# Kernel optimization log

Measured on AMD Instinct MI355X. Metric: run time of the kernel, lower is better.

The kernel has to match this reference:

```python
import jax, jax.numpy as jnp
import numpy as np

T, B, N_INP, N_HID, N_OUT = 512, 128, 256, 1024, 128


def setup_inputs() -> dict:
    key = jax.random.key(0)
    ks = jax.random.split(key, 7)
    x = jax.random.normal(ks[0], (T, B, N_INP), dtype=jnp.float32)
    # PyTorch RNNCell/Linear default init: U(-1/sqrt(fan_in), 1/sqrt(fan_in))
    s_h = 1.0 / np.sqrt(N_HID)
    W_ih = jax.random.uniform(ks[1], (N_HID, N_INP), jnp.float32, -s_h, s_h)
    W_hh = jax.random.uniform(ks[2], (N_HID, N_HID), jnp.float32, -s_h, s_h)
    b_ih = jax.random.uniform(ks[3], (N_HID,), jnp.float32, -s_h, s_h)
    b_hh = jax.random.uniform(ks[4], (N_HID,), jnp.float32, -s_h, s_h)
    W_ro = jax.random.uniform(ks[5], (N_OUT, N_HID), jnp.float32, -s_h, s_h)
    b_ro = jax.random.uniform(ks[6], (N_OUT,), jnp.float32, -s_h, s_h)
    return {"x": x, "W_ih": W_ih, "W_hh": W_hh, "b_ih": b_ih,
            "b_hh": b_hh, "W_ro": W_ro, "b_ro": b_ro}


def reference(x, W_ih, W_hh, b_ih, b_hh, W_ro, b_ro):
    # x: [T, B, n_inp]; recurrence: state = tanh(x_t W_ih^T + b_ih + state W_hh^T + b_hh)
    batch = x.shape[1]
    n_hid = W_hh.shape[0]
    state0 = jnp.zeros((batch, n_hid), dtype=x.dtype)

    # Precompute the input projection for all timesteps in one big GEMM.
    x_proj = jnp.einsum('tbi,hi->tbh', x, W_ih) + b_ih + b_hh  # [T, B, n_hid]

    def step(state, xp_t):
        new_state = jnp.tanh(xp_t + state @ W_hh.T)
        return new_state, None

    final_state, _ = jax.lax.scan(step, state0, x_proj)
    # readout applied to final hidden state only (stateOnly=None path)
    return final_state @ W_ro.T + b_ro  # [B, n_out]
```

## Files before the change

### kernel.cpp

```cpp
#include <hip/hip_runtime.h>
#include <hip/hip_bf16.h>
#include <stdint.h>


#define TSTEPS 512
#define BATCH  128
#define NI     256
#define NH     1024
#define NO     128
#define NBLK   64
#define NTHR   512
#define NWAVE  8
#define BG     16
#define COLS   128

typedef __attribute__((ext_vector_type(8))) short s16x8;
typedef __attribute__((ext_vector_type(4))) float f32x4;
typedef __attribute__((ext_vector_type(4))) unsigned u32x4;
typedef unsigned long long ull;

__device__ __forceinline__ unsigned short f2bf_rne(float f) {
  unsigned u = __builtin_bit_cast(unsigned, f);
  unsigned r = u + 0x7fffu + ((u >> 16) & 1u);
  return (unsigned short)(r >> 16);
}
__device__ __forceinline__ float bf2f(unsigned short h) {
  unsigned u = ((unsigned)h) << 16;
  return __builtin_bit_cast(float, u);
}
__device__ __forceinline__ void split_bf(float v, short &hi, short &lo) {
  unsigned short h = f2bf_rne(v);
  hi = (short)h;
  lo = (short)f2bf_rne(v - bf2f(h));
}
__device__ __forceinline__ f32x4 mfma16(s16x8 a, s16x8 b, f32x4 c) {
  return __builtin_amdgcn_mfma_f32_16x16x32_bf16(a, b, c, 0, 0, 0);
}
__device__ __forceinline__ float fast_tanh(float a) {
  float cl = fminf(fmaxf(a, -15.f), 15.f);
  float e  = __expf(2.f * cl);
  return (e - 1.f) / (e + 1.f);
}

#define SIDX(g, p, r, k) ((((size_t)(g) * NWAVE + (p)) * BG + (r)) * 128 + (k))

__global__ __launch_bounds__(NTHR, 2)
void rnn_persistent(const float* __restrict__ x,
                    const float* __restrict__ W_ih,
                    const float* __restrict__ W_hh,
                    const float* __restrict__ b_ih,
                    const float* __restrict__ b_hh,
                    unsigned*    __restrict__ SP)
{
  const int tid  = threadIdx.x;
  const int wave = tid >> 6;
  const int lane = tid & 63;
  const int lr   = lane & 15;
  const int lq   = lane >> 4;
  const int g    = blockIdx.x & 7;
  const int p    = blockIdx.x >> 3;
  const int row0 = g * BG;
  const int h0   = p * COLS;
  const int kq0  = wave * 128;
  const int iq0  = wave * 32;

  __shared__ float red[NWAVE][BG][COLS];

  s16x8 whh[8][4];
  #pragma unroll
  for (int nt = 0; nt < 8; ++nt) {
    const int h = h0 + nt * 16 + lr;
    #pragma unroll
    for (int kb = 0; kb < 4; ++kb) {
      const float* pw = W_hh + (size_t)h * NH + kq0 + kb * 32 + lq * 8;
      s16x8 hi;
      #pragma unroll
      for (int j = 0; j < 8; ++j) hi[j] = (short)f2bf_rne(pw[j]);
      whh[nt][kb] = hi;
    }
  }
  s16x8 wih[8];
  #pragma unroll
  for (int nt = 0; nt < 8; ++nt) {
    const int h = h0 + nt * 16 + lr;
    const float* pw = W_ih + (size_t)h * NI + iq0 + lq * 8;
    s16x8 hi;
    #pragma unroll
    for (int j = 0; j < 8; ++j) hi[j] = (short)f2bf_rne(pw[j]);
    wih[nt] = hi;
  }

  const int er = tid >> 5;
  const int ec = (tid & 31) * 4;
  float bias[4];
  #pragma unroll
  for (int j = 0; j < 4; ++j) bias[j] = b_ih[h0 + ec + j] + b_hh[h0 + ec + j];

  unsigned* buf0 = SP;
  unsigned* buf1 = SP + (size_t)BATCH * NH;

  float xf[8];
  {
    const float* xp = x + (size_t)(row0 + lr) * NI + iq0 + lq * 8;
    #pragma unroll
    for (int j = 0; j < 8; ++j) xf[j] = xp[j];
  }

  const unsigned* sb0 = buf0 + SIDX(g, wave, lr, lq * 8);
  const unsigned* sb1 = buf1 + SIDX(g, wave, lr, lq * 8);

  for (int t = 0; t < TSTEPS; ++t) {
    f32x4 acc[8];
    #pragma unroll
    for (int nt = 0; nt < 8; ++nt) acc[nt] = (f32x4){0.f, 0.f, 0.f, 0.f};
    {
      s16x8 xhi, xlo;
      #pragma unroll
      for (int j = 0; j < 8; ++j) { short a, b; split_bf(xf[j], a, b); xhi[j] = a; xlo[j] = b; }
      #pragma unroll
      for (int nt = 0; nt < 8; ++nt) {
        acc[nt] = mfma16(xhi, wih[nt], acc[nt]);
        acc[nt] = mfma16(xlo, wih[nt], acc[nt]);
      }
    }
    const unsigned etag = (unsigned)((t >> 1) & 1);
    const unsigned* sb = (t & 1) ? sb1 : sb0;
    u32x4 sv0, sv1, sv2, sv3, sv4, sv5, sv6, sv7;
    {
      const u32x4 e4 = (u32x4){etag, etag, etag, etag};
      for (;;) {
        asm volatile(
          "global_load_dwordx4 %0, %8, off sc1\n\t"
          "global_load_dwordx4 %1, %8, off offset:16 sc1\n\t"
          "global_load_dwordx4 %2, %8, off offset:128 sc1\n\t"
          "global_load_dwordx4 %3, %8, off offset:144 sc1\n\t"
          "global_load_dwordx4 %4, %8, off offset:256 sc1\n\t"
          "global_load_dwordx4 %5, %8, off offset:272 sc1\n\t"
          "global_load_dwordx4 %6, %8, off offset:384 sc1\n\t"
          "global_load_dwordx4 %7, %8, off offset:400 sc1\n\t"
          "s_waitcnt vmcnt(0)"
          : "=&v"(sv0), "=&v"(sv1), "=&v"(sv2), "=&v"(sv3),
            "=&v"(sv4), "=&v"(sv5), "=&v"(sv6), "=&v"(sv7)
          : "v"(sb) : "memory");
        u32x4 b4 = (sv0 ^ e4) | (sv1 ^ e4) | (sv2 ^ e4) | (sv3 ^ e4)
                 | (sv4 ^ e4) | (sv5 ^ e4) | (sv6 ^ e4) | (sv7 ^ e4);
        unsigned bad = b4[0] | b4[1] | b4[2] | b4[3];
        if ((bad & 1u) == 0) break;
      }
    }
    {
      const int tn = (t + 1 < TSTEPS) ? (t + 1) : t;
      const float* xp = x + (size_t)tn * BATCH * NI + (size_t)(row0 + lr) * NI + iq0 + lq * 8;
      #pragma unroll
      for (int j = 0; j < 8; ++j) xf[j] = xp[j];
    }
    #pragma unroll
    for (int kb = 0; kb < 4; ++kb) {
      const u32x4 va = (kb == 0) ? sv0 : (kb == 1) ? sv2 : (kb == 2) ? sv4 : sv6;
      const u32x4 vb = (kb == 0) ? sv1 : (kb == 1) ? sv3 : (kb == 2) ? sv5 : sv7;
      s16x8 shi, slo;
      #pragma unroll
      for (int i = 0; i < 4; ++i) {
        unsigned wa = va[i], wb = vb[i];
        shi[i]     = (short)(wa >> 16); slo[i]     = (short)(wa & 0xffffu);
        shi[i + 4] = (short)(wb >> 16); slo[i + 4] = (short)(wb & 0xffffu);
      }
      #pragma unroll
      for (int nt = 0; nt < 8; ++nt) {
        acc[nt] = mfma16(shi, whh[nt][kb], acc[nt]);
        acc[nt] = mfma16(slo, whh[nt][kb], acc[nt]);
      }
    }
    __syncthreads();
    #pragma unroll
    for (int nt = 0; nt < 8; ++nt)
      #pragma unroll
      for (int r = 0; r < 4; ++r)
        red[wave][lq * 4 + r][nt * 16 + lr] = acc[nt][r];
    __syncthreads();
    {
      float s[4] = {bias[0], bias[1], bias[2], bias[3]};
      #pragma unroll
      for (int w = 0; w < NWAVE; ++w) {
        const f32x4 v = *(const f32x4*)&red[w][er][ec];
        s[0] += v[0]; s[1] += v[1]; s[2] += v[2]; s[3] += v[3];
      }
      const unsigned otag = (unsigned)(((t + 1) >> 1) & 1);
      unsigned pkw[4];
      #pragma unroll
      for (int j = 0; j < 4; ++j) {
        float tv = fast_tanh(s[j]);
        unsigned short hb = f2bf_rne(tv);
        unsigned       lb = ((f2bf_rne(tv - bf2f(hb)) & 0xfffeu) | otag);
        pkw[j] = (((unsigned)hb) << 16) | lb;
      }
      ull pk01 = ((ull)pkw[1] << 32) | (ull)pkw[0];
      ull pk23 = ((ull)pkw[3] << 32) | (ull)pkw[2];
      ull* op = (ull*)(((t + 1) & 1 ? buf1 : buf0) + SIDX(g, p, er, ec));
      __hip_atomic_store(op,     pk01, __ATOMIC_RELAXED, __HIP_MEMORY_SCOPE_AGENT);
      __hip_atomic_store(op + 1, pk23, __ATOMIC_RELAXED, __HIP_MEMORY_SCOPE_AGENT);
    }
  }
}

__global__ __launch_bounds__(256)
void init_buf1(unsigned* __restrict__ SP) {
  const int i = blockIdx.x * 256 + threadIdx.x;
  SP[BATCH * NH + i] = 1u;
}

__global__ __launch_bounds__(512)
void rnn_readout(const unsigned* __restrict__ SP,
                 const float* __restrict__ W_ro,
                 const float* __restrict__ b_ro,
                 float* __restrict__ out)
{
  __shared__ float srow[4][NH];
  const int b0 = blockIdx.x * 4;
  for (int i = threadIdx.x; i < 4 * NH; i += 512) {
    const int b = b0 + (i >> 10);
    const int h = i & 1023;
    unsigned u = SP[SIDX(b >> 4, h >> 7, b & 15, h & 127)];
    srow[i >> 10][h] = bf2f((unsigned short)(u >> 16)) + bf2f((unsigned short)(u & 0xffffu));
  }
  __syncthreads();
  const int bb = threadIdx.x >> 7;
  const int o  = threadIdx.x & 127;
  const float* wr = W_ro + (size_t)o * NH;
  float s = 0.f;
  #pragma unroll 4
  for (int k = 0; k < NH; ++k) s += srow[bb][k] * wr[k];
  out[(size_t)(b0 + bb) * NO + o] = s + b_ro[o];
}

extern "C" void kernel_launch(void* const* d_in, const int* in_sizes, int n_in,
                              void* d_out, int out_size, void* d_ws, size_t ws_size,
                              hipStream_t stream) {
  (void)in_sizes; (void)n_in; (void)out_size; (void)ws_size;
  const float* x    = (const float*)d_in[0];
  const float* W_ih = (const float*)d_in[1];
  const float* W_hh = (const float*)d_in[2];
  const float* b_ih = (const float*)d_in[3];
  const float* b_hh = (const float*)d_in[4];
  const float* W_ro = (const float*)d_in[5];
  const float* b_ro = (const float*)d_in[6];
  float* out = (float*)d_out;

  unsigned* SP = (unsigned*)d_ws;

  hipMemsetAsync(SP, 0, (size_t)BATCH * NH * sizeof(unsigned), stream);
  init_buf1<<<(BATCH * NH) / 256, 256, 0, stream>>>(SP);

  rnn_persistent<<<NBLK, NTHR, 0, stream>>>(x, W_ih, W_hh, b_ih, b_hh, SP);
  rnn_readout<<<BATCH / 4, 512, 0, stream>>>(SP, W_ro, b_ro, out);
}
```

Before: 2.177 ms.

## Mirror hidden state into two buffers with different cache scopes for faster polling

Result: slower. 2.444 ms (+12.3%).

```diff
diff --git a/kernel.cpp b/kernel.cpp
--- a/kernel.cpp
+++ b/kernel.cpp
@@ -13,6 +13,7 @@
 #define NWAVE  8
 #define BG     16
 #define COLS   128
+#define SPBUF  ((size_t)BATCH * NH)
 
 typedef __attribute__((ext_vector_type(8))) short s16x8;
 typedef __attribute__((ext_vector_type(4))) float f32x4;
@@ -44,7 +45,7 @@
 
 #define SIDX(g, p, r, k) ((((size_t)(g) * NWAVE + (p)) * BG + (r)) * 128 + (k))
 
-__global__ __launch_bounds__(NTHR, 2)
+__global__ __launch_bounds__(NTHR, 1)
 void rnn_persistent(const float* __restrict__ x,
                     const float* __restrict__ W_ih,
                     const float* __restrict__ W_hh,
@@ -96,8 +97,10 @@
   #pragma unroll
   for (int j = 0; j < 4; ++j) bias[j] = b_ih[h0 + ec + j] + b_hh[h0 + ec + j];
 
-  unsigned* buf0 = SP;
-  unsigned* buf1 = SP + (size_t)BATCH * NH;
+  unsigned* lb0 = SP;
+  unsigned* lb1 = SP + SPBUF;
+  unsigned* mr0 = SP + 2 * SPBUF;
+  unsigned* mr1 = SP + 3 * SPBUF;
 
   float xf[8];
   {
@@ -106,8 +109,10 @@
     for (int j = 0; j < 8; ++j) xf[j] = xp[j];
   }
 
-  const unsigned* sb0 = buf0 + SIDX(g, wave, lr, lq * 8);
-  const unsigned* sb1 = buf1 + SIDX(g, wave, lr, lq * 8);
+  const size_t soff = SIDX(g, wave, lr, lq * 8);
+  const unsigned* sbL[2] = { lb0 + soff, lb1 + soff };
+  const unsigned* sbM[2] = { mr0 + soff, mr1 + soff };
+  const size_t poff = SIDX(g, p, er, ec);
 
   for (int t = 0; t < TSTEPS; ++t) {
     f32x4 acc[8];
@@ -124,11 +129,31 @@
       }
     }
     const unsigned etag = (unsigned)((t >> 1) & 1);
-    const unsigned* sb = (t & 1) ? sb1 : sb0;
+    const unsigned* sb = sbL[t & 1];
+    const unsigned* mb = sbM[t & 1];
     u32x4 sv0, sv1, sv2, sv3, sv4, sv5, sv6, sv7;
     {
       const u32x4 e4 = (u32x4){etag, etag, etag, etag};
       for (;;) {
+        asm volatile(
+          "global_load_dwordx4 %0, %8, off sc0\n\t"
+          "global_load_dwordx4 %1, %8, off offset:16 sc0\n\t"
+          "global_load_dwordx4 %2, %8, off offset:128 sc0\n\t"
+          "global_load_dwordx4 %3, %8, off offset:144 sc0\n\t"
+          "global_load_dwordx4 %4, %8, off offset:256 sc0\n\t"
+          "global_load_dwordx4 %5, %8, off offset:272 sc0\n\t"
+          "global_load_dwordx4 %6, %8, off offset:384 sc0\n\t"
+          "global_load_dwordx4 %7, %8, off offset:400 sc0\n\t"
+          "s_waitcnt vmcnt(0)"
+          : "=&v"(sv0), "=&v"(sv1), "=&v"(sv2), "=&v"(sv3),
+            "=&v"(sv4), "=&v"(sv5), "=&v"(sv6), "=&v"(sv7)
+          : "v"(sb) : "memory");
+        {
+          u32x4 b4 = (sv0 ^ e4) | (sv1 ^ e4) | (sv2 ^ e4) | (sv3 ^ e4)
+                   | (sv4 ^ e4) | (sv5 ^ e4) | (sv6 ^ e4) | (sv7 ^ e4);
+          unsigned bad = b4[0] | b4[1] | b4[2] | b4[3];
+          if ((bad & 1u) == 0) break;
+        }
         asm volatile(
           "global_load_dwordx4 %0, %8, off sc1\n\t"
           "global_load_dwordx4 %1, %8, off offset:16 sc1\n\t"
@@ -141,11 +166,13 @@
           "s_waitcnt vmcnt(0)"
           : "=&v"(sv0), "=&v"(sv1), "=&v"(sv2), "=&v"(sv3),
             "=&v"(sv4), "=&v"(sv5), "=&v"(sv6), "=&v"(sv7)
-          : "v"(sb) : "memory");
-        u32x4 b4 = (sv0 ^ e4) | (sv1 ^ e4) | (sv2 ^ e4) | (sv3 ^ e4)
-                 | (sv4 ^ e4) | (sv5 ^ e4) | (sv6 ^ e4) | (sv7 ^ e4);
-        unsigned bad = b4[0] | b4[1] | b4[2] | b4[3];
-        if ((bad & 1u) == 0) break;
+          : "v"(mb) : "memory");
+        {
+          u32x4 b4 = (sv0 ^ e4) | (sv1 ^ e4) | (sv2 ^ e4) | (sv3 ^ e4)
+                   | (sv4 ^ e4) | (sv5 ^ e4) | (sv6 ^ e4) | (sv7 ^ e4);
+          unsigned bad = b4[0] | b4[1] | b4[2] | b4[3];
+          if ((bad & 1u) == 0) break;
+        }
       }
     }
     {
@@ -186,7 +213,7 @@
         s[0] += v[0]; s[1] += v[1]; s[2] += v[2]; s[3] += v[3];
       }
       const unsigned otag = (unsigned)(((t + 1) >> 1) & 1);
-      unsigned pkw[4];
+      u32x4 pkw;
       #pragma unroll
       for (int j = 0; j < 4; ++j) {
         float tv = fast_tanh(s[j]);
@@ -194,19 +221,20 @@
         unsigned       lb = ((f2bf_rne(tv - bf2f(hb)) & 0xfffeu) | otag);
         pkw[j] = (((unsigned)hb) << 16) | lb;
       }
-      ull pk01 = ((ull)pkw[1] << 32) | (ull)pkw[0];
-      ull pk23 = ((ull)pkw[3] << 32) | (ull)pkw[2];
-      ull* op = (ull*)(((t + 1) & 1 ? buf1 : buf0) + SIDX(g, p, er, ec));
-      __hip_atomic_store(op,     pk01, __ATOMIC_RELAXED, __HIP_MEMORY_SCOPE_AGENT);
-      __hip_atomic_store(op + 1, pk23, __ATOMIC_RELAXED, __HIP_MEMORY_SCOPE_AGENT);
+      unsigned* lbd = ((t + 1) & 1) ? lb1 : lb0;
+      unsigned* mrd = ((t + 1) & 1) ? mr1 : mr0;
+      unsigned* opL = lbd + poff;
+      unsigned* opM = mrd + poff;
+      asm volatile("global_store_dwordx4 %0, %1, off sc0" :: "v"(opL), "v"(pkw) : "memory");
+      asm volatile("global_store_dwordx4 %0, %1, off sc1" :: "v"(opM), "v"(pkw) : "memory");
     }
   }
 }
 
 __global__ __launch_bounds__(256)
-void init_buf1(unsigned* __restrict__ SP) {
-  const int i = blockIdx.x * 256 + threadIdx.x;
-  SP[BATCH * NH + i] = 1u;
+void init_sp(unsigned* __restrict__ SP) {
+  const size_t i = (size_t)blockIdx.x * 256 + threadIdx.x;
+  SP[i] = (unsigned)((i >> 17) & 1);
 }
 
 __global__ __launch_bounds__(512)
@@ -216,12 +244,13 @@
                  float* __restrict__ out)
 {
   __shared__ float srow[4][NH];
+  const unsigned* MIR0 = SP + 2 * SPBUF;
   const int b0 = blockIdx.x * 4;
   for (int i = threadIdx.x; i < 4 * NH; i += 512) {
     const int b = b0 + (i >> 10);
     const int h = i & 1023;
-    unsigned u = SP[SIDX(b >> 4, h >> 7, b & 15, h & 127)];
-    srow[i >> 10][h] = bf2f((unsigned short)(u >> 16)) + bf2f((unsigned short)(u & 0xffffu));
+    unsigned u = MIR0[SIDX(b >> 4, h >> 7, b & 15, h & 127)];
+    srow[i >> 10][h] = bf2f((unsigned short)(u >> 16)) + bf2f((unsigned short)(u & 0xfffeu));
   }
   __syncthreads();
   const int bb = threadIdx.x >> 7;
@@ -248,8 +277,7 @@
 
   unsigned* SP = (unsigned*)d_ws;
 
-  hipMemsetAsync(SP, 0, (size_t)BATCH * NH * sizeof(unsigned), stream);
-  init_buf1<<<(BATCH * NH) / 256, 256, 0, stream>>>(SP);
+  init_sp<<<(4 * BATCH * NH) / 256, 256, 0, stream>>>(SP);
 
   rnn_persistent<<<NBLK, NTHR, 0, stream>>>(x, W_ih, W_hh, b_ih, b_hh, SP);
   rnn_readout<<<BATCH / 4, 512, 0, stream>>>(SP, W_ro, b_ro, out);
```
